# Optimization experiments

Hardware: AMD Instinct MI355X
Metric: run time of the kernel (lower is better)

## Reference

```python
import jax, jax.numpy as jnp
import numpy as np

B, C, W = 16, 512, 4096
HEADS, HEAD_DIM, GROUPS = 8, 64, 32
HIDDEN = HEADS * HEAD_DIM
EPS = 1e-5


def setup_inputs() -> dict:
    key = jax.random.key(0)
    ks = jax.random.split(key, 3)
    x = jax.random.normal(ks[0], (B, C, W), dtype=jnp.float32)
    # conv1x1 weights (out_ch, in_ch); init scaled like PyTorch kaiming-uniform-ish
    w_qkv = jax.random.normal(ks[1], (3 * HIDDEN, C), dtype=jnp.float32) / np.sqrt(C)
    w_out = jax.random.normal(ks[2], (C, HIDDEN), dtype=jnp.float32) / np.sqrt(HIDDEN)
    return {
        "x": x,
        "gn_w": jnp.ones((C,), jnp.float32),
        "gn_b": jnp.zeros((C,), jnp.float32),
        "w_qkv": w_qkv,
        "b_qkv": jnp.zeros((3 * HIDDEN,), jnp.float32),
        "w_out": w_out,
        "b_out": jnp.zeros((C,), jnp.float32),
    }


def reference(x, gn_w, gn_b, w_qkv, b_qkv, w_out, b_out):
    b, c, w = x.shape
    # GroupNorm over (channels_per_group, width)
    xg = x.reshape(b, GROUPS, -1)
    mu = xg.mean(axis=-1, keepdims=True)
    var = xg.var(axis=-1, keepdims=True)  # biased, matches torch GroupNorm
    xn = ((xg - mu) * jax.lax.rsqrt(var + EPS)).reshape(b, c, w)
    xn = xn * gn_w[None, :, None] + gn_b[None, :, None]
    # 1x1 conv -> qkv
    qkv = jnp.einsum('bcw,oc->bow', xn, w_qkv) + b_qkv[None, :, None]
    qkv = qkv.reshape(b, 3, HEADS, HEAD_DIM, w)
    q, k, v = qkv[:, 0], qkv[:, 1], qkv[:, 2]  # each (b, h, d, n)
    k = jax.nn.softmax(k, axis=-1)  # softmax over sequence positions
    # linear attention: small (d, e) context per head, then project onto q
    context = jnp.einsum('bhdn,bhen->bhde', k, v)
    out = jnp.einsum('bhde,bhdn->bhen', context, q)  # (b, h, d, n)
    out = out.reshape(b, HIDDEN, w)
    return jnp.einsum('bcw,oc->bow', out, w_out) + b_out[None, :, None]
```

## Files before the change

### kernel.cpp

```cpp
#include <hip/hip_runtime.h>
#include <hip/hip_bf16.h>

#define B 16
#define C 512
#define W 4096
#define HEADS 8
#define HD 64
#define GROUPS 32
#define HIDDEN 512
#define OUT3 1536
#define CPG 16
#define GSIZE (CPG * W)
#define EPS 1e-5f

using bf16 = __hip_bfloat16;
typedef __attribute__((ext_vector_type(8))) short short8;
typedef __attribute__((ext_vector_type(4))) float f32x4;

__device__ __forceinline__ float bf_lo(unsigned u) { return __uint_as_float(u << 16); }
__device__ __forceinline__ float bf_hi(unsigned u) { return __uint_as_float(u & 0xffff0000u); }
__device__ __forceinline__ unsigned short f2bf(float f) {
    unsigned u = __float_as_uint(f);
    unsigned r = 0x7fffu + ((u >> 16) & 1u);
    return (unsigned short)((u + r) >> 16);
}
__device__ __forceinline__ unsigned pack2(float a, float b) {
    return (unsigned)f2bf(a) | ((unsigned)f2bf(b) << 16);
}

__device__ __forceinline__ void async16(const ushort* g, ushort* l) {
    __builtin_amdgcn_global_load_lds((const __attribute__((address_space(1))) void*)g,
                                     (__attribute__((address_space(3))) void*)l, 16, 0, 0);
}

#define SBAR                                  \
    do {                                      \
        asm volatile("" ::: "memory");        \
        __builtin_amdgcn_s_barrier();         \
        asm volatile("" ::: "memory");        \
    } while (0)

#define FMA16(a, bb)                                                                      \
    acc[0][0] += a.x * bb.x; acc[0][1] += a.x * bb.y; acc[0][2] += a.x * bb.z; acc[0][3] += a.x * bb.w; \
    acc[1][0] += a.y * bb.x; acc[1][1] += a.y * bb.y; acc[1][2] += a.y * bb.z; acc[1][3] += a.y * bb.w; \
    acc[2][0] += a.z * bb.x; acc[2][1] += a.z * bb.y; acc[2][2] += a.z * bb.z; acc[2][3] += a.z * bb.w; \
    acc[3][0] += a.w * bb.x; acc[3][1] += a.w * bb.y; acc[3][2] += a.w * bb.z; acc[3][3] += a.w * bb.w;

__global__ __launch_bounds__(256) void gn_stats_kernel(const float* __restrict__ x,
                                                       float2* __restrict__ stats) {
    __shared__ float s1[256], s2[256];
    int bg = blockIdx.x;
    const float4* p4 = (const float4*)(x + (size_t)bg * GSIZE);
    float sum = 0.f, sq = 0.f;
    for (int i = threadIdx.x; i < GSIZE / 4; i += 256) {
        float4 u = p4[i];
        sum += u.x + u.y + u.z + u.w;
        sq += u.x * u.x + u.y * u.y + u.z * u.z + u.w * u.w;
    }
    s1[threadIdx.x] = sum; s2[threadIdx.x] = sq;
    __syncthreads();
    for (int st = 128; st > 0; st >>= 1) {
        if (threadIdx.x < st) {
            s1[threadIdx.x] += s1[threadIdx.x + st];
            s2[threadIdx.x] += s2[threadIdx.x + st];
        }
        __syncthreads();
    }
    if (threadIdx.x == 0) {
        float mean = s1[0] / (float)GSIZE;
        float var = s2[0] / (float)GSIZE - mean * mean;
        stats[bg] = make_float2(mean, rsqrtf(var + EPS));
    }
}

__global__ __launch_bounds__(256) void convw_kernel(const float* __restrict__ s,
                                                    ushort* __restrict__ d, int n4) {
    int i = blockIdx.x * 256 + threadIdx.x;
    if (i >= n4) return;
    float4 v = ((const float4*)s)[i];
    ushort4 o; o.x = f2bf(v.x); o.y = f2bf(v.y); o.z = f2bf(v.z); o.w = f2bf(v.w);
    ((ushort4*)d)[i] = o;
}

__global__ __launch_bounds__(256) void conv_xnt_kernel(
    const float* __restrict__ x, const float* __restrict__ gnw, const float* __restrict__ gnb,
    const float2* __restrict__ stats, ushort* __restrict__ xnT) {
    __shared__ ushort tile[64][68];
    int b = blockIdx.z, c0 = blockIdx.y * 64, w0 = blockIdx.x * 64;
    int t = threadIdx.x;
    int rc = t >> 4, rw = (t & 15) * 4;
#pragma unroll
    for (int p = 0; p < 4; p++) {
        int cl = p * 16 + rc;
        int c = c0 + cl;
        float2 st = stats[b * GROUPS + (c >> 4)];
        float gw = gnw[c], gb = gnb[c];
        float scale = st.y * gw;
        float shift = gb - st.x * scale;
        float4 v = *(const float4*)(x + ((size_t)b * C + c) * W + w0 + rw);
        tile[cl][rw + 0] = f2bf(v.x * scale + shift);
        tile[cl][rw + 1] = f2bf(v.y * scale + shift);
        tile[cl][rw + 2] = f2bf(v.z * scale + shift);
        tile[cl][rw + 3] = f2bf(v.w * scale + shift);
    }
    __syncthreads();
#pragma unroll
    for (int p = 0; p < 4; p++) {
        int wl = p * 16 + rc;
        int cl = (t & 15) * 4;
        ushort4 o;
        o.x = tile[cl + 0][wl]; o.y = tile[cl + 1][wl];
        o.z = tile[cl + 2][wl]; o.w = tile[cl + 3][wl];
        *(ushort4*)(xnT + ((size_t)b * W + w0 + wl) * C + c0 + cl) = o;
    }
}

template <bool BF16_OUT>
__global__ __launch_bounds__(512, 2) void gemm256_kernel(
    const ushort* __restrict__ A, const ushort* __restrict__ Bw,
    const float* __restrict__ bias, void* __restrict__ Dv,
    long aBatch, long dBatch) {
    __shared__ ushort sm[65536];
    const int b = blockIdx.z;
    const int m0 = blockIdx.x * 256, n0 = blockIdx.y * 256;
    const ushort* Ab = A + (size_t)b * aBatch;
    const int t = threadIdx.x;
    const int lane = t & 63, wid = t >> 6;
    const int wm = wid >> 2, wn = wid & 3;
    const int quad = lane >> 4, lr = lane & 15;

    auto STAGE = [&](const ushort* P, int row0, int kt, int bb, int isB, int h) {
#pragma unroll
        for (int l = 0; l < 2; l++) {
            int f = t + 512 * l;
            int r = f & 127, kq = f >> 7;
            async16(P + (size_t)(row0 + h * 128 + r) * 512 + kt * 64 + kq * 8,
                    &sm[bb * 32768 + isB * 16384 + h * 1024 + kq * 2048 + r * 8]);
        }
    };

    const int NT = 8;
    STAGE(Bw, n0, 0, 0, 1, 0); STAGE(Bw, n0, 0, 0, 1, 1);
    STAGE(Ab, m0, 0, 0, 0, 0); STAGE(Ab, m0, 0, 0, 0, 1);
    STAGE(Bw, n0, 1, 1, 1, 0); STAGE(Bw, n0, 1, 1, 1, 1);
    STAGE(Ab, m0, 1, 1, 0, 0);
    asm volatile("s_waitcnt vmcnt(6)" ::: "memory");
    SBAR;

    f32x4 acc[8][4] = {};
    for (int kt = 0; kt < NT; kt++) {
        const int bb = kt & 1;
        const ushort* Al = &sm[bb * 32768];
        const ushort* Bl = &sm[bb * 32768 + 16384];
        short8 af[8], bf[8];
#pragma unroll
        for (int j = 0; j < 4; j++) {
            bf[j * 2 + 0] = *(const short8*)&Bl[((0 + quad) * 256 + wn * 64 + j * 16 + lr) * 8];
            bf[j * 2 + 1] = *(const short8*)&Bl[((4 + quad) * 256 + wn * 64 + j * 16 + lr) * 8];
        }
#pragma unroll
        for (int i = 0; i < 8; i++)
            af[i] = *(const short8*)&Al[((0 + quad) * 256 + wm * 128 + i * 16 + lr) * 8];
        if (kt + 1 < NT) STAGE(Ab, m0, kt + 1, bb ^ 1, 0, 1);
        SBAR;
        __builtin_amdgcn_s_setprio(1);
#pragma unroll
        for (int i = 0; i < 8; i++) {
            acc[i][0] = __builtin_amdgcn_mfma_f32_16x16x32_bf16(af[i], bf[0], acc[i][0], 0, 0, 0);
            acc[i][1] = __builtin_amdgcn_mfma_f32_16x16x32_bf16(af[i], bf[2], acc[i][1], 0, 0, 0);
        }
        __builtin_amdgcn_s_setprio(0);
        asm volatile("s_waitcnt lgkmcnt(0)" ::: "memory");
        SBAR;
        if (kt + 2 < NT) STAGE(Bw, n0, kt + 2, bb, 1, 0);
        SBAR;
        __builtin_amdgcn_s_setprio(1);
#pragma unroll
        for (int i = 0; i < 8; i++) {
            acc[i][2] = __builtin_amdgcn_mfma_f32_16x16x32_bf16(af[i], bf[4], acc[i][2], 0, 0, 0);
            acc[i][3] = __builtin_amdgcn_mfma_f32_16x16x32_bf16(af[i], bf[6], acc[i][3], 0, 0, 0);
        }
        __builtin_amdgcn_s_setprio(0);
        SBAR;
#pragma unroll
        for (int i = 0; i < 8; i++)
            af[i] = *(const short8*)&Al[((4 + quad) * 256 + wm * 128 + i * 16 + lr) * 8];
        if (kt + 2 < NT) STAGE(Bw, n0, kt + 2, bb, 1, 1);
        SBAR;
        __builtin_amdgcn_s_setprio(1);
#pragma unroll
        for (int i = 0; i < 8; i++) {
            acc[i][0] = __builtin_amdgcn_mfma_f32_16x16x32_bf16(af[i], bf[1], acc[i][0], 0, 0, 0);
            acc[i][1] = __builtin_amdgcn_mfma_f32_16x16x32_bf16(af[i], bf[3], acc[i][1], 0, 0, 0);
        }
        __builtin_amdgcn_s_setprio(0);
        SBAR;
        if (kt + 2 < NT) STAGE(Ab, m0, kt + 2, bb, 0, 0);
        SBAR;
        __builtin_amdgcn_s_setprio(1);
#pragma unroll
        for (int i = 0; i < 8; i++) {
            acc[i][2] = __builtin_amdgcn_mfma_f32_16x16x32_bf16(af[i], bf[5], acc[i][2], 0, 0, 0);
            acc[i][3] = __builtin_amdgcn_mfma_f32_16x16x32_bf16(af[i], bf[7], acc[i][3], 0, 0, 0);
        }
        __builtin_amdgcn_s_setprio(0);
        if (kt + 2 < NT) {
            asm volatile("s_waitcnt vmcnt(6)" ::: "memory");
        } else {
            asm volatile("s_waitcnt vmcnt(0)" ::: "memory");
        }
        SBAR;
    }

    if constexpr (BF16_OUT) {
        ushort* Db = (ushort*)Dv + (size_t)b * dBatch;
#pragma unroll
        for (int i = 0; i < 8; i++) {
            int mb = m0 + wm * 128 + i * 16 + quad * 4;
#pragma unroll
            for (int j = 0; j < 4; j++) {
                int n = n0 + wn * 64 + j * 16 + lr;
                float bv = bias[n];
                f32x4 v = acc[i][j];
                uint2 st;
                st.x = pack2(v.x + bv, v.y + bv);
                st.y = pack2(v.z + bv, v.w + bv);
                *(uint2*)(Db + (size_t)n * W + mb) = st;
            }
        }
    } else {
        float* Db = (float*)Dv + (size_t)b * dBatch;
#pragma unroll
        for (int i = 0; i < 8; i++) {
            int mb = m0 + wm * 128 + i * 16 + quad * 4;
#pragma unroll
            for (int j = 0; j < 4; j++) {
                int n = n0 + wn * 64 + j * 16 + lr;
                float bv = bias[n];
                f32x4 v = acc[i][j];
                float4 st = make_float4(v.x + bv, v.y + bv, v.z + bv, v.w + bv);
                *(float4*)(Db + (size_t)n * W + mb) = st;
            }
        }
    }
}

__global__ __launch_bounds__(256) void kstats_kernel(const ushort* __restrict__ qkv,
                                                     float2* __restrict__ kst,
                                                     float* __restrict__ ctx) {
    __shared__ float sbuf[256];
    int row = blockIdx.x;
    int t = threadIdx.x;
    if (t < 64) ctx[(size_t)row * 64 + t] = 0.f;
    int b = row >> 9, r = row & 511;
    const uint4* base = (const uint4*)(qkv + ((size_t)b * OUT3 + HIDDEN + r) * W);
    uint4 u0 = base[t];
    uint4 u1 = base[256 + t];
    float v[16];
    v[0] = bf_lo(u0.x); v[1] = bf_hi(u0.x); v[2] = bf_lo(u0.y); v[3] = bf_hi(u0.y);
    v[4] = bf_lo(u0.z); v[5] = bf_hi(u0.z); v[6] = bf_lo(u0.w); v[7] = bf_hi(u0.w);
    v[8] = bf_lo(u1.x); v[9] = bf_hi(u1.x); v[10] = bf_lo(u1.y); v[11] = bf_hi(u1.y);
    v[12] = bf_lo(u1.z); v[13] = bf_hi(u1.z); v[14] = bf_lo(u1.w); v[15] = bf_hi(u1.w);
    float m = v[0];
#pragma unroll
    for (int i = 1; i < 16; i++) m = fmaxf(m, v[i]);
    sbuf[t] = m; __syncthreads();
    for (int st = 128; st > 0; st >>= 1) {
        if (t < st) sbuf[t] = fmaxf(sbuf[t], sbuf[t + st]);
        __syncthreads();
    }
    m = sbuf[0]; __syncthreads();
    float s = 0.f;
#pragma unroll
    for (int i = 0; i < 16; i++) s += __expf(v[i] - m);
    sbuf[t] = s; __syncthreads();
    for (int st = 128; st > 0; st >>= 1) {
        if (t < st) sbuf[t] += sbuf[t + st];
        __syncthreads();
    }
    if (t == 0) kst[row] = make_float2(m, 1.0f / sbuf[0]);
}

__global__ __launch_bounds__(256) void kv_context_kernel(const ushort* __restrict__ qkv,
                                                         const float2* __restrict__ kst,
                                                         float* __restrict__ ctx) {
    __shared__ float kS[64][68];
    __shared__ float vS[64][68];
    int bh = blockIdx.y;
    int b = bh >> 3, h = bh & 7;
    int nbase = blockIdx.x * 512;
    const ushort* kbase = qkv + ((size_t)b * OUT3 + HIDDEN + h * HD) * W;
    const ushort* vbase = qkv + ((size_t)b * OUT3 + 2 * HIDDEN + h * HD) * W;
    int t = threadIdx.x, tx = t & 15, ty = t >> 4;
    int lr = t >> 4, lc = (t & 15) * 4;
    float acc[4][4] = {};
    for (int n0 = nbase; n0 < nbase + 512; n0 += 64) {
#pragma unroll
        for (int rr = 0; rr < 4; rr++) {
            int row = lr + rr * 16;
            float m = kst[b * HIDDEN + h * HD + row].x;
            const unsigned* kp = (const unsigned*)(kbase + (size_t)row * W + n0 + lc);
            unsigned k0 = kp[0], k1 = kp[1];
            kS[lc + 0][row] = __expf(bf_lo(k0) - m);
            kS[lc + 1][row] = __expf(bf_hi(k0) - m);
            kS[lc + 2][row] = __expf(bf_lo(k1) - m);
            kS[lc + 3][row] = __expf(bf_hi(k1) - m);
            const unsigned* vp = (const unsigned*)(vbase + (size_t)row * W + n0 + lc);
            unsigned v0 = vp[0], v1 = vp[1];
            vS[lc + 0][row] = bf_lo(v0); vS[lc + 1][row] = bf_hi(v0);
            vS[lc + 2][row] = bf_lo(v1); vS[lc + 3][row] = bf_hi(v1);
        }
        __syncthreads();
#pragma unroll 8
        for (int n = 0; n < 64; n++) {
            float4 a = *(const float4*)&kS[n][ty * 4];
            float4 bb = *(const float4*)&vS[n][tx * 4];
            FMA16(a, bb)
        }
        __syncthreads();
    }
#pragma unroll
    for (int i = 0; i < 4; i++)
#pragma unroll
        for (int j = 0; j < 4; j++)
            atomicAdd(&ctx[((size_t)bh * 64 + ty * 4 + i) * 64 + tx * 4 + j], acc[i][j]);
}

__global__ __launch_bounds__(256) void apply_context_kernel(const ushort* __restrict__ qkv,
                                                            const float* __restrict__ ctx,
                                                            const float2* __restrict__ kst,
                                                            ushort* __restrict__ attnT) {
    __shared__ float cS[64][68];
    __shared__ float qS[64][68];
    int bh = blockIdx.y;
    int b = bh >> 3, h = bh & 7;
    int n0 = blockIdx.x * 64;
    const ushort* qbase = qkv + ((size_t)b * OUT3 + h * HD) * W;
    int t = threadIdx.x, tx = t & 15, ty = t >> 4;
    int lr = t >> 4, lc = (t & 15) * 4;
#pragma unroll
    for (int rr = 0; rr < 4; rr++) {
        int row = lr + rr * 16;
        float inv = kst[b * HIDDEN + h * HD + row].y;
        float4 cv = *(const float4*)(ctx + ((size_t)bh * 64 + row) * 64 + lc);
        cv.x *= inv; cv.y *= inv; cv.z *= inv; cv.w *= inv;
        *(float4*)&cS[row][lc] = cv;
        const unsigned* qp = (const unsigned*)(qbase + (size_t)row * W + n0 + lc);
        unsigned q0 = qp[0], q1 = qp[1];
        *(float4*)&qS[row][lc] = make_float4(bf_lo(q0), bf_hi(q0), bf_lo(q1), bf_hi(q1));
    }
    __syncthreads();
    float acc[4][4] = {};
#pragma unroll 8
    for (int d = 0; d < 64; d++) {
        float4 a = *(const float4*)&qS[d][ty * 4];
        float4 bb = *(const float4*)&cS[d][tx * 4];
        FMA16(a, bb)
    }
#pragma unroll
    for (int i = 0; i < 4; i++) {
        int w = n0 + ty * 4 + i;
        uint2 st;
        st.x = pack2(acc[i][0], acc[i][1]);
        st.y = pack2(acc[i][2], acc[i][3]);
        *(uint2*)(attnT + ((size_t)b * W + w) * HIDDEN + h * HD + tx * 4) = st;
    }
}

extern "C" void kernel_launch(void* const* d_in, const int* in_sizes, int n_in,
                              void* d_out, int out_size, void* d_ws, size_t ws_size,
                              hipStream_t stream) {
    const float* x   = (const float*)d_in[0];
    const float* gnw = (const float*)d_in[1];
    const float* gnb = (const float*)d_in[2];
    const float* wq  = (const float*)d_in[3];
    const float* bq  = (const float*)d_in[4];
    const float* wo  = (const float*)d_in[5];
    const float* bo  = (const float*)d_in[6];
    float* out = (float*)d_out;

    char* ws = (char*)d_ws;
    ushort* qkv   = (ushort*)ws;
    ushort* xnT   = (ushort*)(ws + 201326592ull);
    ushort* attnT = xnT;
    char*   r256  = ws + 268435456ull;
    ushort* wqb   = (ushort*)r256;
    float*  ctx   = (float*)r256;
    float2* stats = (float2*)(ws + 270532608ull);
    ushort* wob   = qkv;
    float2* kst   = (float2*)d_out;

    gn_stats_kernel<<<B * GROUPS, 256, 0, stream>>>(x, stats);
    convw_kernel<<<(OUT3 * C / 4 + 255) / 256, 256, 0, stream>>>(wq, wqb, OUT3 * C / 4);
    conv_xnt_kernel<<<dim3(W / 64, C / 64, B), 256, 0, stream>>>(x, gnw, gnb, stats, xnT);
    gemm256_kernel<true><<<dim3(W / 256, OUT3 / 256, B), 512, 0, stream>>>(
        xnT, wqb, bq, qkv, (long)W * C, (long)OUT3 * W);
    kstats_kernel<<<B * HIDDEN, 256, 0, stream>>>(qkv, kst, ctx);
    kv_context_kernel<<<dim3(8, B * HEADS), 256, 0, stream>>>(qkv, kst, ctx);
    apply_context_kernel<<<dim3(W / 64, B * HEADS), 256, 0, stream>>>(qkv, ctx, kst, attnT);
    convw_kernel<<<(C * HIDDEN / 4 + 255) / 256, 256, 0, stream>>>(wo, wob, C * HIDDEN / 4);
    gemm256_kernel<false><<<dim3(W / 256, C / 256, B), 512, 0, stream>>>(
        attnT, wob, bo, out, (long)W * HIDDEN, (long)C * W);
}
```

Baseline: 645.9 us.

## Fold linear-attention context into per-batch output weights and use MFMA for KV context

The attention context, scaled by the softmax normalisation, is folded into the output projection. A per-batch effective weight W_eff = w_out·ctxᵀ is built, and the second GEMM reads Q directly, so the apply_context pass and the attnT intermediate are gone. The key softmax stats and the KV context are merged into one MFMA-based kernel that computes exp(k) without subtracting the row max and accumulates the row sums alongside. The QKV GEMM epilogue now writes Q position-major with scalar 2-byte stores, which coalesce poorly. Dropping the max subtraction risks overflow for large key values.

```diff
diff --git a/kernel.cpp b/kernel.cpp
--- a/kernel.cpp
+++ b/kernel.cpp
@@ -19,6 +19,7 @@
 
 __device__ __forceinline__ float bf_lo(unsigned u) { return __uint_as_float(u << 16); }
 __device__ __forceinline__ float bf_hi(unsigned u) { return __uint_as_float(u & 0xffff0000u); }
+__device__ __forceinline__ float bf2f(unsigned short s) { return __uint_as_float(((unsigned)s) << 16); }
 __device__ __forceinline__ unsigned short f2bf(float f) {
     unsigned u = __float_as_uint(f);
     unsigned r = 0x7fffu + ((u >> 16) & 1u);
@@ -39,12 +40,6 @@
         __builtin_amdgcn_s_barrier();         \
         asm volatile("" ::: "memory");        \
     } while (0)
-
-#define FMA16(a, bb)                                                                      \
-    acc[0][0] += a.x * bb.x; acc[0][1] += a.x * bb.y; acc[0][2] += a.x * bb.z; acc[0][3] += a.x * bb.w; \
-    acc[1][0] += a.y * bb.x; acc[1][1] += a.y * bb.y; acc[1][2] += a.y * bb.z; acc[1][3] += a.y * bb.w; \
-    acc[2][0] += a.z * bb.x; acc[2][1] += a.z * bb.y; acc[2][2] += a.z * bb.z; acc[2][3] += a.z * bb.w; \
-    acc[3][0] += a.w * bb.x; acc[3][1] += a.w * bb.y; acc[3][2] += a.w * bb.z; acc[3][3] += a.w * bb.w;
 
 __global__ __launch_bounds__(256) void gn_stats_kernel(const float* __restrict__ x,
                                                        float2* __restrict__ stats) {
@@ -119,11 +114,12 @@
 __global__ __launch_bounds__(512, 2) void gemm256_kernel(
     const ushort* __restrict__ A, const ushort* __restrict__ Bw,
     const float* __restrict__ bias, void* __restrict__ Dv,
-    long aBatch, long dBatch) {
+    long aBatch, long dBatch, long bBatch) {
     __shared__ ushort sm[65536];
     const int b = blockIdx.z;
     const int m0 = blockIdx.x * 256, n0 = blockIdx.y * 256;
     const ushort* Ab = A + (size_t)b * aBatch;
+    const ushort* Bwb = Bw + (size_t)b * bBatch;
     const int t = threadIdx.x;
     const int lane = t & 63, wid = t >> 6;
     const int wm = wid >> 2, wn = wid & 3;
@@ -140,9 +136,9 @@
     };
 
     const int NT = 8;
-    STAGE(Bw, n0, 0, 0, 1, 0); STAGE(Bw, n0, 0, 0, 1, 1);
+    STAGE(Bwb, n0, 0, 0, 1, 0); STAGE(Bwb, n0, 0, 0, 1, 1);
     STAGE(Ab, m0, 0, 0, 0, 0); STAGE(Ab, m0, 0, 0, 0, 1);
-    STAGE(Bw, n0, 1, 1, 1, 0); STAGE(Bw, n0, 1, 1, 1, 1);
+    STAGE(Bwb, n0, 1, 1, 1, 0); STAGE(Bwb, n0, 1, 1, 1, 1);
     STAGE(Ab, m0, 1, 1, 0, 0);
     asm volatile("s_waitcnt vmcnt(6)" ::: "memory");
     SBAR;
@@ -172,7 +168,7 @@
         __builtin_amdgcn_s_setprio(0);
         asm volatile("s_waitcnt lgkmcnt(0)" ::: "memory");
         SBAR;
-        if (kt + 2 < NT) STAGE(Bw, n0, kt + 2, bb, 1, 0);
+        if (kt + 2 < NT) STAGE(Bwb, n0, kt + 2, bb, 1, 0);
         SBAR;
         __builtin_amdgcn_s_setprio(1);
 #pragma unroll
@@ -185,7 +181,7 @@
 #pragma unroll
         for (int i = 0; i < 8; i++)
             af[i] = *(const short8*)&Al[((4 + quad) * 256 + wm * 128 + i * 16 + lr) * 8];
-        if (kt + 2 < NT) STAGE(Bw, n0, kt + 2, bb, 1, 1);
+        if (kt + 2 < NT) STAGE(Bwb, n0, kt + 2, bb, 1, 1);
         SBAR;
         __builtin_amdgcn_s_setprio(1);
 #pragma unroll
@@ -214,18 +210,34 @@
 
     if constexpr (BF16_OUT) {
         ushort* Db = (ushort*)Dv + (size_t)b * dBatch;
-#pragma unroll
-        for (int i = 0; i < 8; i++) {
-            int mb = m0 + wm * 128 + i * 16 + quad * 4;
-#pragma unroll
-            for (int j = 0; j < 4; j++) {
-                int n = n0 + wn * 64 + j * 16 + lr;
-                float bv = bias[n];
-                f32x4 v = acc[i][j];
-                uint2 st;
-                st.x = pack2(v.x + bv, v.y + bv);
-                st.y = pack2(v.z + bv, v.w + bv);
-                *(uint2*)(Db + (size_t)n * W + mb) = st;
+        if (n0 < HIDDEN) {
+#pragma unroll
+            for (int i = 0; i < 8; i++) {
+                int mb = m0 + wm * 128 + i * 16 + quad * 4;
+#pragma unroll
+                for (int j = 0; j < 4; j++) {
+                    int n = n0 + wn * 64 + j * 16 + lr;
+                    float bv = bias[n];
+                    f32x4 v = acc[i][j];
+#pragma unroll
+                    for (int r = 0; r < 4; r++)
+                        Db[(size_t)(mb + r) * HIDDEN + n] = f2bf(v[r] + bv);
+                }
+            }
+        } else {
+#pragma unroll
+            for (int i = 0; i < 8; i++) {
+                int mb = m0 + wm * 128 + i * 16 + quad * 4;
+#pragma unroll
+                for (int j = 0; j < 4; j++) {
+                    int n = n0 + wn * 64 + j * 16 + lr;
+                    float bv = bias[n];
+                    f32x4 v = acc[i][j];
+                    uint2 st;
+                    st.x = pack2(v.x + bv, v.y + bv);
+                    st.y = pack2(v.z + bv, v.w + bv);
+                    *(uint2*)(Db + (size_t)n * W + mb) = st;
+                }
             }
         }
     } else {
@@ -245,125 +257,127 @@
     }
 }
 
-__global__ __launch_bounds__(256) void kstats_kernel(const ushort* __restrict__ qkv,
-                                                     float2* __restrict__ kst,
-                                                     float* __restrict__ ctx) {
-    __shared__ float sbuf[256];
-    int row = blockIdx.x;
-    int t = threadIdx.x;
-    if (t < 64) ctx[(size_t)row * 64 + t] = 0.f;
-    int b = row >> 9, r = row & 511;
-    const uint4* base = (const uint4*)(qkv + ((size_t)b * OUT3 + HIDDEN + r) * W);
-    uint4 u0 = base[t];
-    uint4 u1 = base[256 + t];
-    float v[16];
-    v[0] = bf_lo(u0.x); v[1] = bf_hi(u0.x); v[2] = bf_lo(u0.y); v[3] = bf_hi(u0.y);
-    v[4] = bf_lo(u0.z); v[5] = bf_hi(u0.z); v[6] = bf_lo(u0.w); v[7] = bf_hi(u0.w);
-    v[8] = bf_lo(u1.x); v[9] = bf_hi(u1.x); v[10] = bf_lo(u1.y); v[11] = bf_hi(u1.y);
-    v[12] = bf_lo(u1.z); v[13] = bf_hi(u1.z); v[14] = bf_lo(u1.w); v[15] = bf_hi(u1.w);
-    float m = v[0];
-#pragma unroll
-    for (int i = 1; i < 16; i++) m = fmaxf(m, v[i]);
-    sbuf[t] = m; __syncthreads();
-    for (int st = 128; st > 0; st >>= 1) {
-        if (t < st) sbuf[t] = fmaxf(sbuf[t], sbuf[t + st]);
-        __syncthreads();
-    }
-    m = sbuf[0]; __syncthreads();
-    float s = 0.f;
-#pragma unroll
-    for (int i = 0; i < 16; i++) s += __expf(v[i] - m);
-    sbuf[t] = s; __syncthreads();
-    for (int st = 128; st > 0; st >>= 1) {
-        if (t < st) sbuf[t] += sbuf[t + st];
-        __syncthreads();
-    }
-    if (t == 0) kst[row] = make_float2(m, 1.0f / sbuf[0]);
-}
-
-__global__ __launch_bounds__(256) void kv_context_kernel(const ushort* __restrict__ qkv,
-                                                         const float2* __restrict__ kst,
-                                                         float* __restrict__ ctx) {
-    __shared__ float kS[64][68];
-    __shared__ float vS[64][68];
-    int bh = blockIdx.y;
+#define LOADKV(KR, VR, n0_)                                                                  \
+    {                                                                                        \
+        _Pragma("unroll") for (int i = 0; i < 4; i++) {                                      \
+            KR[i] = *(const uint4*)(kbase + (size_t)(i * 16 + lr) * W + (n0_) + quad * 8);   \
+            VR[i] = *(const uint4*)(vbase + (size_t)(i * 16 + lr) * W + (n0_) + quad * 8);   \
+        }                                                                                    \
+    }
+#define STEPKV(KR, VR)                                                                       \
+    {                                                                                        \
+        short8 af[4], bfv[4];                                                                \
+        _Pragma("unroll") for (int i = 0; i < 4; i++) {                                      \
+            uint4 u = KR[i];                                                                 \
+            float e0 = __expf(bf_lo(u.x)), e1 = __expf(bf_hi(u.x));                          \
+            float e2 = __expf(bf_lo(u.y)), e3 = __expf(bf_hi(u.y));                          \
+            float e4 = __expf(bf_lo(u.z)), e5 = __expf(bf_hi(u.z));                          \
+            float e6 = __expf(bf_lo(u.w)), e7 = __expf(bf_hi(u.w));                          \
+            psum[i] += e0 + e1 + e2 + e3 + e4 + e5 + e6 + e7;                                \
+            uint4 pk;                                                                        \
+            pk.x = pack2(e0, e1); pk.y = pack2(e2, e3);                                      \
+            pk.z = pack2(e4, e5); pk.w = pack2(e6, e7);                                      \
+            af[i] = *(short8*)&pk;                                                           \
+            bfv[i] = *(short8*)&VR[i];                                                       \
+        }                                                                                    \
+        _Pragma("unroll") for (int i = 0; i < 4; i++)                                        \
+            _Pragma("unroll") for (int j = 0; j < 4; j++)                                    \
+                acc[i][j] = __builtin_amdgcn_mfma_f32_16x16x32_bf16(af[i], bfv[j],           \
+                                                                    acc[i][j], 0, 0, 0);     \
+    }
+
+__global__ __launch_bounds__(512) void kv_ctx_kernel(const ushort* __restrict__ qkv,
+                                                     float* __restrict__ ctx,
+                                                     float* __restrict__ sums) {
+    __shared__ float ctxS[64][68];
+    __shared__ float ssum[64];
+    int bh = blockIdx.x;
     int b = bh >> 3, h = bh & 7;
-    int nbase = blockIdx.x * 512;
     const ushort* kbase = qkv + ((size_t)b * OUT3 + HIDDEN + h * HD) * W;
     const ushort* vbase = qkv + ((size_t)b * OUT3 + 2 * HIDDEN + h * HD) * W;
-    int t = threadIdx.x, tx = t & 15, ty = t >> 4;
-    int lr = t >> 4, lc = (t & 15) * 4;
-    float acc[4][4] = {};
-    for (int n0 = nbase; n0 < nbase + 512; n0 += 64) {
-#pragma unroll
-        for (int rr = 0; rr < 4; rr++) {
-            int row = lr + rr * 16;
-            float m = kst[b * HIDDEN + h * HD + row].x;
-            const unsigned* kp = (const unsigned*)(kbase + (size_t)row * W + n0 + lc);
-            unsigned k0 = kp[0], k1 = kp[1];
-            kS[lc + 0][row] = __expf(bf_lo(k0) - m);
-            kS[lc + 1][row] = __expf(bf_hi(k0) - m);
-            kS[lc + 2][row] = __expf(bf_lo(k1) - m);
-            kS[lc + 3][row] = __expf(bf_hi(k1) - m);
-            const unsigned* vp = (const unsigned*)(vbase + (size_t)row * W + n0 + lc);
-            unsigned v0 = vp[0], v1 = vp[1];
-            vS[lc + 0][row] = bf_lo(v0); vS[lc + 1][row] = bf_hi(v0);
-            vS[lc + 2][row] = bf_lo(v1); vS[lc + 3][row] = bf_hi(v1);
-        }
-        __syncthreads();
-#pragma unroll 8
-        for (int n = 0; n < 64; n++) {
-            float4 a = *(const float4*)&kS[n][ty * 4];
-            float4 bb = *(const float4*)&vS[n][tx * 4];
-            FMA16(a, bb)
-        }
-        __syncthreads();
-    }
+    int t = threadIdx.x, lane = t & 63, wv = t >> 6;
+    int quad = lane >> 4, lr = lane & 15;
+
+    for (int i = t; i < 64 * 68; i += 512) ((float*)ctxS)[i] = 0.f;
+    if (t < 64) ssum[t] = 0.f;
+    __syncthreads();
+
+    const int nbase = wv * 512;
+    f32x4 acc[4][4] = {};
+    float psum[4] = {0.f, 0.f, 0.f, 0.f};
+    uint4 ka[4], va[4], kb[4], vb[4];
+
+    LOADKV(ka, va, nbase);
+    for (int s = 0; s < 16; s += 2) {
+        if (s + 1 < 16) LOADKV(kb, vb, nbase + (s + 1) * 32);
+        STEPKV(ka, va);
+        if (s + 2 < 16) LOADKV(ka, va, nbase + (s + 2) * 32);
+        STEPKV(kb, vb);
+    }
+
 #pragma unroll
     for (int i = 0; i < 4; i++)
 #pragma unroll
-        for (int j = 0; j < 4; j++)
-            atomicAdd(&ctx[((size_t)bh * 64 + ty * 4 + i) * 64 + tx * 4 + j], acc[i][j]);
-}
-
-__global__ __launch_bounds__(256) void apply_context_kernel(const ushort* __restrict__ qkv,
-                                                            const float* __restrict__ ctx,
-                                                            const float2* __restrict__ kst,
-                                                            ushort* __restrict__ attnT) {
-    __shared__ float cS[64][68];
-    __shared__ float qS[64][68];
-    int bh = blockIdx.y;
-    int b = bh >> 3, h = bh & 7;
-    int n0 = blockIdx.x * 64;
-    const ushort* qbase = qkv + ((size_t)b * OUT3 + h * HD) * W;
-    int t = threadIdx.x, tx = t & 15, ty = t >> 4;
-    int lr = t >> 4, lc = (t & 15) * 4;
-#pragma unroll
-    for (int rr = 0; rr < 4; rr++) {
-        int row = lr + rr * 16;
-        float inv = kst[b * HIDDEN + h * HD + row].y;
-        float4 cv = *(const float4*)(ctx + ((size_t)bh * 64 + row) * 64 + lc);
-        cv.x *= inv; cv.y *= inv; cv.z *= inv; cv.w *= inv;
-        *(float4*)&cS[row][lc] = cv;
-        const unsigned* qp = (const unsigned*)(qbase + (size_t)row * W + n0 + lc);
-        unsigned q0 = qp[0], q1 = qp[1];
-        *(float4*)&qS[row][lc] = make_float4(bf_lo(q0), bf_hi(q0), bf_lo(q1), bf_hi(q1));
+        for (int j = 0; j < 4; j++) {
+            f32x4 v = acc[i][j];
+#pragma unroll
+            for (int r = 0; r < 4; r++)
+                atomicAdd(&ctxS[i * 16 + quad * 4 + r][j * 16 + lr], v[r]);
+        }
+#pragma unroll
+    for (int i = 0; i < 4; i++) {
+        float v = psum[i];
+        v += __shfl_xor(v, 16);
+        v += __shfl_xor(v, 32);
+        if (quad == 0) atomicAdd(&ssum[i * 16 + lr], v);
     }
     __syncthreads();
-    float acc[4][4] = {};
-#pragma unroll 8
-    for (int d = 0; d < 64; d++) {
-        float4 a = *(const float4*)&qS[d][ty * 4];
-        float4 bb = *(const float4*)&cS[d][tx * 4];
-        FMA16(a, bb)
-    }
-#pragma unroll
-    for (int i = 0; i < 4; i++) {
-        int w = n0 + ty * 4 + i;
-        uint2 st;
-        st.x = pack2(acc[i][0], acc[i][1]);
-        st.y = pack2(acc[i][2], acc[i][3]);
-        *(uint2*)(attnT + ((size_t)b * W + w) * HIDDEN + h * HD + tx * 4) = st;
+    {
+        int d = t >> 3, e0 = (t & 7) * 8;
+        float4 a = *(const float4*)&ctxS[d][e0];
+        float4 c = *(const float4*)&ctxS[d][e0 + 4];
+        float* dst = ctx + (size_t)bh * 4096 + d * 64 + e0;
+        *(float4*)dst = a;
+        *(float4*)(dst + 4) = c;
+    }
+    if (t < 64) sums[(size_t)bh * 64 + t] = ssum[t];
+}
+
+__global__ __launch_bounds__(256) void weff_kernel(const float* __restrict__ wo,
+                                                   const float* __restrict__ ctx,
+                                                   const float* __restrict__ sums,
+                                                   ushort* __restrict__ weff) {
+    __shared__ ushort woS[128 * 64];
+    __shared__ float ctxS[64][65];
+    int cz = blockIdx.x, h = blockIdx.y, b = blockIdx.z;
+    int bh = b * 8 + h;
+    int t = threadIdx.x;
+    for (int f = t; f < 1024; f += 256) {
+        int d = f >> 4, c4 = (f & 15) * 4;
+        float4 v = *(const float4*)(ctx + (size_t)bh * 4096 + d * 64 + c4);
+        ctxS[d][c4 + 0] = v.x; ctxS[d][c4 + 1] = v.y;
+        ctxS[d][c4 + 2] = v.z; ctxS[d][c4 + 3] = v.w;
+    }
+    for (int f = t; f < 1024; f += 256) {
+        int cl = f >> 3, e8 = (f & 7) * 8;
+        const float4* p = (const float4*)(wo + (size_t)(cz * 128 + cl) * HIDDEN + h * 64 + e8);
+        float4 a = p[0], c = p[1];
+        uint4 pk;
+        pk.x = pack2(a.x, a.y); pk.y = pack2(a.z, a.w);
+        pk.z = pack2(c.x, c.y); pk.w = pack2(c.z, c.w);
+        *(uint4*)&woS[cl * 64 + e8] = pk;
+    }
+    __syncthreads();
+    int d = t & 63, wvq = t >> 6;
+    float pd = 1.0f / sums[(size_t)bh * 64 + d];
+    for (int i = 0; i < 32; i++) {
+        int cl = wvq * 32 + i;
+        float acc = 0.f;
+#pragma unroll
+        for (int e = 0; e < 64; e++)
+            acc += bf2f(woS[cl * 64 + e]) * ctxS[d][e];
+        int c = cz * 128 + cl;
+        weff[(size_t)b * (HIDDEN * HIDDEN) + (size_t)c * HIDDEN + h * 64 + d] = f2bf(acc * pd);
     }
 }
 
@@ -382,23 +396,19 @@
     char* ws = (char*)d_ws;
     ushort* qkv   = (ushort*)ws;
     ushort* xnT   = (ushort*)(ws + 201326592ull);
-    ushort* attnT = xnT;
-    char*   r256  = ws + 268435456ull;
-    ushort* wqb   = (ushort*)r256;
-    float*  ctx   = (float*)r256;
+    ushort* weff  = xnT;
+    float*  sums  = (float*)(ws + 209715200ull);
+    ushort* wqb   = (ushort*)(ws + 268435456ull);
+    float*  ctx   = (float*)(ws + 268435456ull);
     float2* stats = (float2*)(ws + 270532608ull);
-    ushort* wob   = qkv;
-    float2* kst   = (float2*)d_out;
 
     gn_stats_kernel<<<B * GROUPS, 256, 0, stream>>>(x, stats);
     convw_kernel<<<(OUT3 * C / 4 + 255) / 256, 256, 0, stream>>>(wq, wqb, OUT3 * C / 4);
     conv_xnt_kernel<<<dim3(W / 64, C / 64, B), 256, 0, stream>>>(x, gnw, gnb, stats, xnT);
     gemm256_kernel<true><<<dim3(W / 256, OUT3 / 256, B), 512, 0, stream>>>(
-        xnT, wqb, bq, qkv, (long)W * C, (long)OUT3 * W);
-    kstats_kernel<<<B * HIDDEN, 256, 0, stream>>>(qkv, kst, ctx);
-    kv_context_kernel<<<dim3(8, B * HEADS), 256, 0, stream>>>(qkv, kst, ctx);
-    apply_context_kernel<<<dim3(W / 64, B * HEADS), 256, 0, stream>>>(qkv, ctx, kst, attnT);
-    convw_kernel<<<(C * HIDDEN / 4 + 255) / 256, 256, 0, stream>>>(wo, wob, C * HIDDEN / 4);
+        xnT, wqb, bq, qkv, (long)W * C, (long)OUT3 * W, 0L);
+    kv_ctx_kernel<<<B * HEADS, 512, 0, stream>>>(qkv, ctx, sums);
+    weff_kernel<<<dim3(4, HEADS, B), 256, 0, stream>>>(wo, ctx, sums, weff);
     gemm256_kernel<false><<<dim3(W / 256, C / 256, B), 512, 0, stream>>>(
-        attnT, wob, bo, out, (long)W * HIDDEN, (long)C * W);
-}
+        qkv, weff, bo, out, (long)OUT3 * W, (long)C * W, (long)HIDDEN * HIDDEN);
+}
```

Result: faster. 586.1 us (-9.3%).
